# Performance work log

Hardware: AMD Instinct MI355X
Metric: run time of the kernel (lower is better)

The kernel has to match this reference:

```python
import jax, jax.numpy as jnp
import numpy as np

B, N, C1, C2, H = 4, 4096, 320, 256, 5
HD = C1 // H  # 64


def setup_inputs() -> dict:
    key = jax.random.key(0)
    ks = jax.random.split(key, 9)
    w = lambda k, shape, fan_in: jax.random.normal(k, shape, jnp.float32) * (fan_in ** -0.5)
    return {
        "x1": jax.random.normal(ks[0], (B, N, C1), jnp.float32),
        "x2": jax.random.normal(ks[1], (B, N, C2), jnp.float32),
        # nn.Linear weights, torch layout [out_features, in_features]
        "q1_w": w(ks[2], (C1, C1), C1),
        "q2_w": w(ks[3], (C1, C2), C2),
        "kv1_w": w(ks[4], (2 * C1, C2), C2),
        "kv2_w": w(ks[5], (2 * C1, C1), C1),
        "proj1_w": w(ks[6], (C1, C1), C1),
        "proj1_b": jnp.zeros((C1,), jnp.float32),
        "proj2_w": w(ks[7], (C1, C1), C1),
        "proj2_b": jnp.zeros((C1,), jnp.float32),
    }


def _branch(xq, xkv, q_w, kv_w, proj_w, proj_b):
    b, n, _ = xq.shape
    scale = HD ** -0.5
    q = (xq @ q_w.T).reshape(b, n, H, HD).transpose(0, 2, 1, 3)          # [B,H,N,HD]
    kv = (xkv @ kv_w.T).reshape(b, n, 2, H, HD).transpose(2, 0, 3, 1, 4)  # [2,B,H,N,HD]
    k, v = kv[0], kv[1]
    attn = jax.nn.softmax(jnp.einsum('bhqd,bhkd->bhqk', q * scale, k), axis=-1)
    y = jnp.einsum('bhqk,bhkd->bhqd', attn, v)                            # [B,H,N,HD]
    y = y.transpose(0, 2, 1, 3).reshape(b, n, C1)
    return y @ proj_w.T + proj_b


def reference(x1, x2, q1_w, q2_w, kv1_w, kv2_w, proj1_w, proj1_b, proj2_w, proj2_b):
    y1 = _branch(x1, x2, q1_w, kv1_w, proj1_w, proj1_b)  # x1 queries, x2 keys/values
    y2 = _branch(x2, x1, q2_w, kv2_w, proj2_w, proj2_b)  # x2 queries, x1 keys/values
    return jnp.concatenate((y1, y2), axis=-1)            # [B,N,2*C1]
```

## Files before the change

kernel.cpp:

```cpp
#include <hip/hip_runtime.h>
#include <hip/hip_bf16.h>

#define Bb 4
#define Nn 4096
#define C1 320
#define C2 256
#define Hh 5
#define HD 64
#define Mm (Bb*Nn)

using bf16 = __hip_bfloat16;
typedef __attribute__((ext_vector_type(8))) short  short8;
typedef __attribute__((ext_vector_type(4))) short  short4_;
typedef __attribute__((ext_vector_type(4))) float  f32x4;
typedef __attribute__((ext_vector_type(16))) float f32x16;
typedef __attribute__((ext_vector_type(2)))  float f32x2;

__device__ __forceinline__ short f2s(float f) {
    bf16 h = __float2bfloat16(f);
    short s;
    __builtin_memcpy(&s, &h, 2);
    return s;
}

__device__ __forceinline__ float fexp2(float x) {
#if __has_builtin(__builtin_amdgcn_exp2f)
    return __builtin_amdgcn_exp2f(x);
#else
    return exp2f(x);
#endif
}

__device__ __forceinline__ int swz(int row, int bb) {
    return row * 64 + ((bb ^ (row & 7)) << 3);
}
__device__ __forceinline__ int swz16(int row, int bb) {
    return row * 128 + ((bb ^ (row & 7)) << 3);
}

__device__ __forceinline__ unsigned cvtpk(float lo, float hi) {
    unsigned r;
    asm("v_cvt_pk_bf16_f32 %0, %1, %2" : "=v"(r) : "v"(lo), "v"(hi));
    return r;
}

__device__ __forceinline__ f32x2 pkadd(f32x2 a, f32x2 b) {
    f32x2 d;
    asm("v_pk_add_f32 %0, %1, %2" : "=v"(d) : "v"(a), "v"(b));
    return d;
}

__device__ __forceinline__ void plswap(unsigned &a, unsigned &b) {
#if __has_builtin(__builtin_amdgcn_permlane32_swap)
    auto r = __builtin_amdgcn_permlane32_swap(a, b, false, false);
    a = r[0]; b = r[1];
#else
    asm("v_permlane32_swap_b32 %0, %1" : "+v"(a), "+v"(b));
#endif
}

__device__ __forceinline__ short8 mk8(unsigned d0, unsigned d1, unsigned d2, unsigned d3) {
    union { unsigned u[4]; short8 s; } u;
    u.u[0] = d0; u.u[1] = d1; u.u[2] = d2; u.u[3] = d3;
    return u.s;
}

struct CvtArgs {
    const float* s[8];
    bf16* d[8];
    int off[9];
};

__global__ void cvt_all(CvtArgs a) {
    int i = (blockIdx.x * blockDim.x + threadIdx.x) * 4;
    if (i >= a.off[8]) return;
    int seg = 0;
    #pragma unroll
    for (int k = 1; k < 8; ++k) seg += (i >= a.off[k]);
    int j = i - a.off[seg];
    float4 v = *(const float4*)(a.s[seg] + j);
    short4_ o = { f2s(v.x), f2s(v.y), f2s(v.z), f2s(v.w) };
    *(short4_*)(a.d[seg] + j) = o;
}

__global__ __launch_bounds__(256) void gemm_proj(
    const bf16* __restrict__ A1, const bf16* __restrict__ Wq1, const bf16* __restrict__ Wkv1,
    const bf16* __restrict__ A2, const bf16* __restrict__ Wq2, const bf16* __restrict__ Wkv2,
    float qs,
    bf16* __restrict__ Qo1, bf16* __restrict__ Ko1, bf16* __restrict__ Vo1,
    bf16* __restrict__ Qo2, bf16* __restrict__ Ko2, bf16* __restrict__ Vo2)
{
    __shared__ bf16 la[128 * 64];
    __shared__ bf16 lw[64 * 64];
    const int m0 = blockIdx.x * 128;
    const int by = blockIdx.y;
    const int g = (by >= 15);
    const int yy = by - 15 * g;
    const int K = g ? C2 : C1;
    const bf16* A = g ? A2 : A1;
    const bool isq = yy < 5;
    const bf16* W = isq ? (g ? Wq2 : Wq1) : (g ? Wkv2 : Wkv1);
    bf16* Qo = g ? Qo2 : Qo1;
    bf16* Ko = g ? Ko2 : Ko1;
    bf16* Vo = g ? Vo2 : Vo1;
    const int n0 = (isq ? yy : yy - 5) * 64;
    const int t = threadIdx.x;
    const int wave = t >> 6, lane = t & 63, l16 = lane & 15, quad = lane >> 4;
    const int sr = t >> 3, sb = t & 7;

    f32x4 acc[2][4];
    #pragma unroll
    for (int mf = 0; mf < 2; ++mf)
        #pragma unroll
        for (int nt = 0; nt < 4; ++nt) acc[mf][nt] = {0.f,0.f,0.f,0.f};

    const int nk = K >> 6;
    const bf16* ap = A + (size_t)(m0 + sr) * K + sb * 8;
    const bf16* wp = W + (size_t)(n0 + sr) * K + sb * 8;
    short8 ra0 = *(const short8*)ap;
    short8 ra1 = *(const short8*)(ap + (size_t)32 * K);
    short8 ra2 = *(const short8*)(ap + (size_t)64 * K);
    short8 ra3 = *(const short8*)(ap + (size_t)96 * K);
    short8 rw0 = *(const short8*)wp;
    short8 rw1 = *(const short8*)(wp + (size_t)32 * K);

    for (int kt = 0; kt < nk; ++kt) {
        __syncthreads();
        *(short8*)&la[swz(sr,      sb)] = ra0;
        *(short8*)&la[swz(sr + 32, sb)] = ra1;
        *(short8*)&la[swz(sr + 64, sb)] = ra2;
        *(short8*)&la[swz(sr + 96, sb)] = ra3;
        *(short8*)&lw[swz(sr,      sb)] = rw0;
        *(short8*)&lw[swz(sr + 32, sb)] = rw1;
        __syncthreads();
        if (kt + 1 < nk) {
            ap += 64; wp += 64;
            ra0 = *(const short8*)ap;
            ra1 = *(const short8*)(ap + (size_t)32 * K);
            ra2 = *(const short8*)(ap + (size_t)64 * K);
            ra3 = *(const short8*)(ap + (size_t)96 * K);
            rw0 = *(const short8*)wp;
            rw1 = *(const short8*)(wp + (size_t)32 * K);
        }
        const int arow = wave * 32 + l16;
        short8 a00 = *(const short8*)&la[swz(arow,      quad)];
        short8 a01 = *(const short8*)&la[swz(arow,      quad + 4)];
        short8 a10 = *(const short8*)&la[swz(arow + 16, quad)];
        short8 a11 = *(const short8*)&la[swz(arow + 16, quad + 4)];
        #pragma unroll
        for (int nt = 0; nt < 4; ++nt) {
            const int brow = nt * 16 + l16;
            short8 b0 = *(const short8*)&lw[swz(brow, quad)];
            short8 b1 = *(const short8*)&lw[swz(brow, quad + 4)];
            acc[0][nt] = __builtin_amdgcn_mfma_f32_16x16x32_bf16(a00, b0, acc[0][nt], 0, 0, 0);
            acc[0][nt] = __builtin_amdgcn_mfma_f32_16x16x32_bf16(a01, b1, acc[0][nt], 0, 0, 0);
            acc[1][nt] = __builtin_amdgcn_mfma_f32_16x16x32_bf16(a10, b0, acc[1][nt], 0, 0, 0);
            acc[1][nt] = __builtin_amdgcn_mfma_f32_16x16x32_bf16(a11, b1, acc[1][nt], 0, 0, 0);
        }
    }

    const bool isv = !isq && n0 >= C1;
    #pragma unroll
    for (int mf = 0; mf < 2; ++mf) {
        const int mrow = m0 + wave * 32 + mf * 16 + quad * 4;
        if (isq) {
            #pragma unroll
            for (int nt = 0; nt < 4; ++nt) {
                int col = n0 + nt * 16 + l16;
                #pragma unroll
                for (int r = 0; r < 4; ++r)
                    Qo[(size_t)(mrow + r) * C1 + col] = __float2bfloat16(acc[mf][nt][r] * qs);
            }
        } else if (!isv) {
            #pragma unroll
            for (int nt = 0; nt < 4; ++nt) {
                int col = n0 + nt * 16 + l16;
                #pragma unroll
                for (int r = 0; r < 4; ++r)
                    Ko[(size_t)(mrow + r) * C1 + col] = __float2bfloat16(acc[mf][nt][r]);
            }
        } else {
            #pragma unroll
            for (int nt = 0; nt < 4; ++nt) {
                int col = n0 + nt * 16 + l16 - C1;
                int h = col >> 6, d = col & 63;
                #pragma unroll
                for (int r = 0; r < 4; ++r) {
                    int m = mrow + r;
                    int b = m >> 12, n = m & (Nn - 1);
                    Vo[((size_t)(b * Hh + h) * 64 + d) * Nn + n] = __float2bfloat16(acc[mf][nt][r]);
                }
            }
        }
    }
}

__global__ __launch_bounds__(256) void gemm_out(
    const bf16* __restrict__ Y1, const bf16* __restrict__ Wp1, const float* __restrict__ B1,
    const bf16* __restrict__ Y2, const bf16* __restrict__ Wp2, const float* __restrict__ B2,
    float* __restrict__ Of)
{
    __shared__ bf16 la[128 * 64];
    __shared__ bf16 lw[64 * 64];
    const int zz = blockIdx.z;
    const bf16* A = zz ? Y2 : Y1;
    const bf16* W = zz ? Wp2 : Wp1;
    const float* bias = zz ? B2 : B1;
    const int ooff = zz ? C1 : 0;
    const int m0 = blockIdx.x * 128, n0 = blockIdx.y * 64;
    const int t = threadIdx.x;
    const int wave = t >> 6, lane = t & 63, l16 = lane & 15, quad = lane >> 4;
    const int sr = t >> 3, sb = t & 7;
    const int K = C1;

    f32x4 acc[2][4];
    #pragma unroll
    for (int mf = 0; mf < 2; ++mf)
        #pragma unroll
        for (int nt = 0; nt < 4; ++nt) acc[mf][nt] = {0.f,0.f,0.f,0.f};

    const int nk = K >> 6;
    const bf16* ap = A + (size_t)(m0 + sr) * K + sb * 8;
    const bf16* wp = W + (size_t)(n0 + sr) * K + sb * 8;
    short8 ra0 = *(const short8*)ap;
    short8 ra1 = *(const short8*)(ap + (size_t)32 * K);
    short8 ra2 = *(const short8*)(ap + (size_t)64 * K);
    short8 ra3 = *(const short8*)(ap + (size_t)96 * K);
    short8 rw0 = *(const short8*)wp;
    short8 rw1 = *(const short8*)(wp + (size_t)32 * K);

    for (int kt = 0; kt < nk; ++kt) {
        __syncthreads();
        *(short8*)&la[swz(sr,      sb)] = ra0;
        *(short8*)&la[swz(sr + 32, sb)] = ra1;
        *(short8*)&la[swz(sr + 64, sb)] = ra2;
        *(short8*)&la[swz(sr + 96, sb)] = ra3;
        *(short8*)&lw[swz(sr,      sb)] = rw0;
        *(short8*)&lw[swz(sr + 32, sb)] = rw1;
        __syncthreads();
        if (kt + 1 < nk) {
            ap += 64; wp += 64;
            ra0 = *(const short8*)ap;
            ra1 = *(const short8*)(ap + (size_t)32 * K);
            ra2 = *(const short8*)(ap + (size_t)64 * K);
            ra3 = *(const short8*)(ap + (size_t)96 * K);
            rw0 = *(const short8*)wp;
            rw1 = *(const short8*)(wp + (size_t)32 * K);
        }
        const int arow = wave * 32 + l16;
        short8 a00 = *(const short8*)&la[swz(arow,      quad)];
        short8 a01 = *(const short8*)&la[swz(arow,      quad + 4)];
        short8 a10 = *(const short8*)&la[swz(arow + 16, quad)];
        short8 a11 = *(const short8*)&la[swz(arow + 16, quad + 4)];
        #pragma unroll
        for (int nt = 0; nt < 4; ++nt) {
            const int brow = nt * 16 + l16;
            short8 b0 = *(const short8*)&lw[swz(brow, quad)];
            short8 b1 = *(const short8*)&lw[swz(brow, quad + 4)];
            acc[0][nt] = __builtin_amdgcn_mfma_f32_16x16x32_bf16(a00, b0, acc[0][nt], 0, 0, 0);
            acc[0][nt] = __builtin_amdgcn_mfma_f32_16x16x32_bf16(a01, b1, acc[0][nt], 0, 0, 0);
            acc[1][nt] = __builtin_amdgcn_mfma_f32_16x16x32_bf16(a10, b0, acc[1][nt], 0, 0, 0);
            acc[1][nt] = __builtin_amdgcn_mfma_f32_16x16x32_bf16(a11, b1, acc[1][nt], 0, 0, 0);
        }
    }

    #pragma unroll
    for (int mf = 0; mf < 2; ++mf) {
        const int mrow = m0 + wave * 32 + mf * 16 + quad * 4;
        #pragma unroll
        for (int nt = 0; nt < 4; ++nt) {
            int col = n0 + nt * 16 + l16;
            float bv = bias[col];
            #pragma unroll
            for (int r = 0; r < 4; ++r)
                Of[(size_t)(mrow + r) * 640 + ooff + col] = acc[mf][nt][r] + bv;
        }
    }
}

__global__ __launch_bounds__(256, 2) void flash_kernel(
    const bf16* __restrict__ Q1, const bf16* __restrict__ K1,
    const bf16* __restrict__ V1, bf16* __restrict__ Y1,
    const bf16* __restrict__ Q2, const bf16* __restrict__ K2,
    const bf16* __restrict__ V2, bf16* __restrict__ Y2)
{
    __shared__ bf16 lk[128 * 64];
    __shared__ bf16 lv[64 * 128];
    const int qt = blockIdx.x, h = blockIdx.y, z = blockIdx.z;
    const int b = z & 3, branch = z >> 2;
    const bf16* Q  = branch ? Q2 : Q1;
    const bf16* Km = branch ? K2 : K1;
    const bf16* Vt = branch ? V2 : V1;
    bf16*       Yo = branch ? Y2 : Y1;

    const int t = threadIdx.x;
    const int wave = t >> 6, lane = t & 63;
    const int l32 = lane & 31, hi = lane >> 5;
    const int sr = t >> 3, sb = t & 7;

    const int qrow0 = qt * 256 + wave * 64;

    short8 qf[2][4];
    #pragma unroll
    for (int qb = 0; qb < 2; ++qb) {
        const bf16* qptr = Q + (size_t)(b * Nn + qrow0 + qb * 32 + l32) * C1 + h * HD + hi * 8;
        #pragma unroll
        for (int ksd = 0; ksd < 4; ++ksd)
            qf[qb][ksd] = *(const short8*)(qptr + ksd * 16);
    }

    f32x16 o[2][2];
    #pragma unroll
    for (int qb = 0; qb < 2; ++qb)
        #pragma unroll
        for (int db = 0; db < 2; ++db)
            o[qb][db] = (f32x16){0.f,0.f,0.f,0.f,0.f,0.f,0.f,0.f,0.f,0.f,0.f,0.f,0.f,0.f,0.f,0.f};
    float lsum[2] = {0.f, 0.f};

    const bf16* Kbase = Km + (size_t)b * Nn * C1 + h * HD;
    const bf16* Vbase = Vt + (size_t)(b * Hh + h) * 64 * Nn;

    const bf16* kp0 = Kbase + (size_t)sr * C1 + sb * 8;
    const bf16* vp0 = Vbase + (size_t)sr * Nn + sb * 8;
    short8 rk0 = *(const short8*)kp0;
    short8 rk1 = *(const short8*)(kp0 + (size_t)32 * C1);
    short8 rk2 = *(const short8*)(kp0 + (size_t)64 * C1);
    short8 rk3 = *(const short8*)(kp0 + (size_t)96 * C1);
    short8 rv0 = *(const short8*)vp0;
    short8 rv1 = *(const short8*)(vp0 + 64);
    short8 rv2 = *(const short8*)(vp0 + (size_t)32 * Nn);
    short8 rv3 = *(const short8*)(vp0 + (size_t)32 * Nn + 64);

    const int NT = Nn / 128;
    for (int kt = 0; kt < NT; ++kt) {
        __syncthreads();
        *(short8*)&lk[swz(sr,      sb)] = rk0;
        *(short8*)&lk[swz(sr + 32, sb)] = rk1;
        *(short8*)&lk[swz(sr + 64, sb)] = rk2;
        *(short8*)&lk[swz(sr + 96, sb)] = rk3;
        *(short8*)&lv[swz16(sr,      sb)]     = rv0;
        *(short8*)&lv[swz16(sr,      sb + 8)] = rv1;
        *(short8*)&lv[swz16(sr + 32, sb)]     = rv2;
        *(short8*)&lv[swz16(sr + 32, sb + 8)] = rv3;
        __syncthreads();
        if (kt + 1 < NT) {
            kp0 += (size_t)128 * C1;
            vp0 += 128;
            rk0 = *(const short8*)kp0;
            rk1 = *(const short8*)(kp0 + (size_t)32 * C1);
            rk2 = *(const short8*)(kp0 + (size_t)64 * C1);
            rk3 = *(const short8*)(kp0 + (size_t)96 * C1);
            rv0 = *(const short8*)vp0;
            rv1 = *(const short8*)(vp0 + 64);
            rv2 = *(const short8*)(vp0 + (size_t)32 * Nn);
            rv3 = *(const short8*)(vp0 + (size_t)32 * Nn + 64);
        }

        #pragma unroll
        for (int kb = 0; kb < 4; ++kb) {
            short8 ka[4];
            #pragma unroll
            for (int ksd = 0; ksd < 4; ++ksd)
                ka[ksd] = *(const short8*)&lk[swz(kb * 32 + l32, ksd * 2 + hi)];

            short8 pa[2][2];
            #pragma unroll
            for (int qb = 0; qb < 2; ++qb) {
                f32x16 s = (f32x16){0.f,0.f,0.f,0.f,0.f,0.f,0.f,0.f,0.f,0.f,0.f,0.f,0.f,0.f,0.f,0.f};
                #pragma unroll
                for (int ksd = 0; ksd < 4; ++ksd)
                    s = __builtin_amdgcn_mfma_f32_32x32x16_bf16(ka[ksd], qf[qb][ksd], s, 0, 0, 0);
                float p[16];
                #pragma unroll
                for (int r = 0; r < 16; ++r) p[r] = fexp2(s[r]);
                {
                    f32x2 t0 = pkadd((f32x2){p[0], p[1]},  (f32x2){p[2], p[3]});
                    f32x2 t1 = pkadd((f32x2){p[4], p[5]},  (f32x2){p[6], p[7]});
                    f32x2 t2 = pkadd((f32x2){p[8], p[9]},  (f32x2){p[10], p[11]});
                    f32x2 t3 = pkadd((f32x2){p[12], p[13]},(f32x2){p[14], p[15]});
                    t0 = pkadd(t0, t1);
                    t2 = pkadd(t2, t3);
                    t0 = pkadd(t0, t2);
                    lsum[qb] += t0.x + t0.y;
                }
                unsigned d0 = cvtpk(p[0],  p[1]),  d2 = cvtpk(p[4],  p[5]);
                plswap(d0, d2);
                unsigned d1 = cvtpk(p[2],  p[3]),  d3 = cvtpk(p[6],  p[7]);
                plswap(d1, d3);
                pa[qb][0] = mk8(d0, d1, d2, d3);
                unsigned e0 = cvtpk(p[8],  p[9]),  e2 = cvtpk(p[12], p[13]);
                plswap(e0, e2);
                unsigned e1 = cvtpk(p[10], p[11]), e3 = cvtpk(p[14], p[15]);
                plswap(e1, e3);
                pa[qb][1] = mk8(e0, e1, e2, e3);
            }

            #pragma unroll
            for (int ks = 0; ks < 2; ++ks) {
                #pragma unroll
                for (int db = 0; db < 2; ++db) {
                    short8 bv = *(const short8*)&lv[swz16(db * 32 + l32, kb * 4 + ks * 2 + hi)];
                    o[0][db] = __builtin_amdgcn_mfma_f32_32x32x16_bf16(pa[0][ks], bv, o[0][db], 0, 0, 0);
                    o[1][db] = __builtin_amdgcn_mfma_f32_32x32x16_bf16(pa[1][ks], bv, o[1][db], 0, 0, 0);
                }
            }
        }
    }

    #pragma unroll
    for (int qb = 0; qb < 2; ++qb) {
        float l = lsum[qb] + __shfl_xor(lsum[qb], 32, 64);
        float inv = 1.0f / l;
        #pragma unroll
        for (int r = 0; r < 16; ++r) {
            const int qr = (r & 3) + 8 * (r >> 2) + 4 * hi;
            float invr = __shfl(inv, qr, 64);
            size_t row = (size_t)(b * Nn + qrow0 + qb * 32 + qr);
            #pragma unroll
            for (int db = 0; db < 2; ++db)
                Yo[row * C1 + h * HD + db * 32 + l32] = __float2bfloat16(o[qb][db][r] * invr);
        }
    }
}

extern "C" void kernel_launch(void* const* d_in, const int* in_sizes, int n_in,
                              void* d_out, int out_size, void* d_ws, size_t ws_size,
                              hipStream_t stream)
{
    const float* x1   = (const float*)d_in[0];
    const float* x2   = (const float*)d_in[1];
    const float* q1w  = (const float*)d_in[2];
    const float* q2w  = (const float*)d_in[3];
    const float* kv1w = (const float*)d_in[4];
    const float* kv2w = (const float*)d_in[5];
    const float* p1w  = (const float*)d_in[6];
    const float* p1b  = (const float*)d_in[7];
    const float* p2w  = (const float*)d_in[8];
    const float* p2b  = (const float*)d_in[9];
    float* out = (float*)d_out;

    bf16* ws = (bf16*)d_ws;
    size_t o = 0;
    bf16* x1b  = ws + o; o += (size_t)Mm * C1;
    bf16* x2b  = ws + o; o += (size_t)Mm * C2;
    bf16* wq1  = ws + o; o += C1 * C1;
    bf16* wq2  = ws + o; o += C1 * C2;
    bf16* wkv1 = ws + o; o += 2 * C1 * C2;
    bf16* wkv2 = ws + o; o += 2 * C1 * C1;
    bf16* wp1  = ws + o; o += C1 * C1;
    bf16* wp2  = ws + o; o += C1 * C1;
    bf16* Q1   = ws + o; o += (size_t)Mm * C1;
    bf16* K1   = ws + o; o += (size_t)Mm * C1;
    bf16* V1t  = ws + o; o += (size_t)Mm * C1;
    bf16* Q2   = ws + o; o += (size_t)Mm * C1;
    bf16* K2   = ws + o; o += (size_t)Mm * C1;
    bf16* V2t  = ws + o; o += (size_t)Mm * C1;
    bf16* Y1   = ws + o; o += (size_t)Mm * C1;
    bf16* Y2   = ws + o; o += (size_t)Mm * C1;
    (void)ws_size; (void)in_sizes; (void)n_in; (void)out_size;

    CvtArgs ca;
    ca.s[0] = x1;   ca.d[0] = x1b;  int n0 = Mm * C1;
    ca.s[1] = x2;   ca.d[1] = x2b;  int n1 = Mm * C2;
    ca.s[2] = q1w;  ca.d[2] = wq1;  int n2 = C1 * C1;
    ca.s[3] = q2w;  ca.d[3] = wq2;  int n3 = C1 * C2;
    ca.s[4] = kv1w; ca.d[4] = wkv1; int n4 = 2 * C1 * C2;
    ca.s[5] = kv2w; ca.d[5] = wkv2; int n5 = 2 * C1 * C1;
    ca.s[6] = p1w;  ca.d[6] = wp1;  int n6 = C1 * C1;
    ca.s[7] = p2w;  ca.d[7] = wp2;  int n7 = C1 * C1;
    int ns[8] = {n0, n1, n2, n3, n4, n5, n6, n7};
    ca.off[0] = 0;
    for (int i = 0; i < 8; ++i) ca.off[i + 1] = ca.off[i] + ns[i];
    int total = ca.off[8];
    cvt_all<<<dim3((total / 4 + 255) / 256), 256, 0, stream>>>(ca);

    const float QS = 0.125f * 1.4426950408889634f;

    gemm_proj<<<dim3(Mm / 128, 30), 256, 0, stream>>>(
        x1b, wq1, wkv2, x2b, wq2, wkv1, QS,
        Q1, K2, V2t, Q2, K1, V1t);

    flash_kernel<<<dim3(Nn / 256, Hh, 2 * Bb), 256, 0, stream>>>(Q1, K1, V1t, Y1, Q2, K2, V2t, Y2);

    gemm_out<<<dim3(Mm / 128, C1 / 64, 2), 256, 0, stream>>>(Y1, wp1, p1b, Y2, wp2, p2b, out);
}
```

Before: 352.2 us.

## Fuse activation fp32-to-bf16 conversion into projection GEMM; shrink flash KV tile

The projection GEMM now loads the fp32 activations directly and converts them to bf16 in registers before the shared-memory store, so the separate conversion pass over x1/x2 and its bf16 workspace copies go away. The conversion kernel now handles only the weights. Separately, the flash attention kernel's K/V tile drops from 128 to 64 keys per iteration, halving shared memory and prefetch registers in exchange for twice as many barrier-synchronised iterations. The GEMM now reads twice as many bytes of A per tile, and because gemm_proj has 30 column blocks per row panel, the fp32 activations are fetched repeatedly at double width.

```diff
diff --git a/kernel.cpp b/kernel.cpp
--- a/kernel.cpp
+++ b/kernel.cpp
@@ -34,9 +34,6 @@
 __device__ __forceinline__ int swz(int row, int bb) {
     return row * 64 + ((bb ^ (row & 7)) << 3);
 }
-__device__ __forceinline__ int swz16(int row, int bb) {
-    return row * 128 + ((bb ^ (row & 7)) << 3);
-}
 
 __device__ __forceinline__ unsigned cvtpk(float lo, float hi) {
     unsigned r;
@@ -65,18 +62,23 @@
     return u.s;
 }
 
+__device__ __forceinline__ short8 cvt8(float4 lo, float4 hi) {
+    return mk8(cvtpk(lo.x, lo.y), cvtpk(lo.z, lo.w),
+               cvtpk(hi.x, hi.y), cvtpk(hi.z, hi.w));
+}
+
 struct CvtArgs {
-    const float* s[8];
-    bf16* d[8];
-    int off[9];
+    const float* s[6];
+    bf16* d[6];
+    int off[7];
 };
 
 __global__ void cvt_all(CvtArgs a) {
     int i = (blockIdx.x * blockDim.x + threadIdx.x) * 4;
-    if (i >= a.off[8]) return;
+    if (i >= a.off[6]) return;
     int seg = 0;
     #pragma unroll
-    for (int k = 1; k < 8; ++k) seg += (i >= a.off[k]);
+    for (int k = 1; k < 6; ++k) seg += (i >= a.off[k]);
     int j = i - a.off[seg];
     float4 v = *(const float4*)(a.s[seg] + j);
     short4_ o = { f2s(v.x), f2s(v.y), f2s(v.z), f2s(v.w) };
@@ -84,8 +86,8 @@
 }
 
 __global__ __launch_bounds__(256) void gemm_proj(
-    const bf16* __restrict__ A1, const bf16* __restrict__ Wq1, const bf16* __restrict__ Wkv1,
-    const bf16* __restrict__ A2, const bf16* __restrict__ Wq2, const bf16* __restrict__ Wkv2,
+    const float* __restrict__ A1, const bf16* __restrict__ Wq1, const bf16* __restrict__ Wkv1,
+    const float* __restrict__ A2, const bf16* __restrict__ Wq2, const bf16* __restrict__ Wkv2,
     float qs,
     bf16* __restrict__ Qo1, bf16* __restrict__ Ko1, bf16* __restrict__ Vo1,
     bf16* __restrict__ Qo2, bf16* __restrict__ Ko2, bf16* __restrict__ Vo2)
@@ -97,7 +99,7 @@
     const int g = (by >= 15);
     const int yy = by - 15 * g;
     const int K = g ? C2 : C1;
-    const bf16* A = g ? A2 : A1;
+    const float* A = g ? A2 : A1;
     const bool isq = yy < 5;
     const bf16* W = isq ? (g ? Wq2 : Wq1) : (g ? Wkv2 : Wkv1);
     bf16* Qo = g ? Qo2 : Qo1;
@@ -115,30 +117,30 @@
         for (int nt = 0; nt < 4; ++nt) acc[mf][nt] = {0.f,0.f,0.f,0.f};
 
     const int nk = K >> 6;
-    const bf16* ap = A + (size_t)(m0 + sr) * K + sb * 8;
-    const bf16* wp = W + (size_t)(n0 + sr) * K + sb * 8;
-    short8 ra0 = *(const short8*)ap;
-    short8 ra1 = *(const short8*)(ap + (size_t)32 * K);
-    short8 ra2 = *(const short8*)(ap + (size_t)64 * K);
-    short8 ra3 = *(const short8*)(ap + (size_t)96 * K);
+    const float* ap = A + (size_t)(m0 + sr) * K + sb * 8;
+    const bf16*  wp = W + (size_t)(n0 + sr) * K + sb * 8;
+    float4 fa0 = *(const float4*)ap,                       fa0h = *(const float4*)(ap + 4);
+    float4 fa1 = *(const float4*)(ap + (size_t)32 * K),    fa1h = *(const float4*)(ap + (size_t)32 * K + 4);
+    float4 fa2 = *(const float4*)(ap + (size_t)64 * K),    fa2h = *(const float4*)(ap + (size_t)64 * K + 4);
+    float4 fa3 = *(const float4*)(ap + (size_t)96 * K),    fa3h = *(const float4*)(ap + (size_t)96 * K + 4);
     short8 rw0 = *(const short8*)wp;
     short8 rw1 = *(const short8*)(wp + (size_t)32 * K);
 
     for (int kt = 0; kt < nk; ++kt) {
         __syncthreads();
-        *(short8*)&la[swz(sr,      sb)] = ra0;
-        *(short8*)&la[swz(sr + 32, sb)] = ra1;
-        *(short8*)&la[swz(sr + 64, sb)] = ra2;
-        *(short8*)&la[swz(sr + 96, sb)] = ra3;
+        *(short8*)&la[swz(sr,      sb)] = cvt8(fa0, fa0h);
+        *(short8*)&la[swz(sr + 32, sb)] = cvt8(fa1, fa1h);
+        *(short8*)&la[swz(sr + 64, sb)] = cvt8(fa2, fa2h);
+        *(short8*)&la[swz(sr + 96, sb)] = cvt8(fa3, fa3h);
         *(short8*)&lw[swz(sr,      sb)] = rw0;
         *(short8*)&lw[swz(sr + 32, sb)] = rw1;
         __syncthreads();
         if (kt + 1 < nk) {
             ap += 64; wp += 64;
-            ra0 = *(const short8*)ap;
-            ra1 = *(const short8*)(ap + (size_t)32 * K);
-            ra2 = *(const short8*)(ap + (size_t)64 * K);
-            ra3 = *(const short8*)(ap + (size_t)96 * K);
+            fa0 = *(const float4*)ap;                    fa0h = *(const float4*)(ap + 4);
+            fa1 = *(const float4*)(ap + (size_t)32 * K); fa1h = *(const float4*)(ap + (size_t)32 * K + 4);
+            fa2 = *(const float4*)(ap + (size_t)64 * K); fa2h = *(const float4*)(ap + (size_t)64 * K + 4);
+            fa3 = *(const float4*)(ap + (size_t)96 * K); fa3h = *(const float4*)(ap + (size_t)96 * K + 4);
             rw0 = *(const short8*)wp;
             rw1 = *(const short8*)(wp + (size_t)32 * K);
         }
@@ -284,8 +286,8 @@
     const bf16* __restrict__ Q2, const bf16* __restrict__ K2,
     const bf16* __restrict__ V2, bf16* __restrict__ Y2)
 {
-    __shared__ bf16 lk[128 * 64];
-    __shared__ bf16 lv[64 * 128];
+    __shared__ bf16 lk[64 * 64];
+    __shared__ bf16 lv[64 * 64];
     const int qt = blockIdx.x, h = blockIdx.y, z = blockIdx.z;
     const int b = z & 3, branch = z >> 2;
     const bf16* Q  = branch ? Q2 : Q1;
@@ -321,43 +323,32 @@
     const bf16* Vbase = Vt + (size_t)(b * Hh + h) * 64 * Nn;
 
     const bf16* kp0 = Kbase + (size_t)sr * C1 + sb * 8;
+    const bf16* kp1 = kp0 + (size_t)32 * C1;
     const bf16* vp0 = Vbase + (size_t)sr * Nn + sb * 8;
+    const bf16* vp1 = vp0 + (size_t)32 * Nn;
     short8 rk0 = *(const short8*)kp0;
-    short8 rk1 = *(const short8*)(kp0 + (size_t)32 * C1);
-    short8 rk2 = *(const short8*)(kp0 + (size_t)64 * C1);
-    short8 rk3 = *(const short8*)(kp0 + (size_t)96 * C1);
+    short8 rk1 = *(const short8*)kp1;
     short8 rv0 = *(const short8*)vp0;
-    short8 rv1 = *(const short8*)(vp0 + 64);
-    short8 rv2 = *(const short8*)(vp0 + (size_t)32 * Nn);
-    short8 rv3 = *(const short8*)(vp0 + (size_t)32 * Nn + 64);
-
-    const int NT = Nn / 128;
+    short8 rv1 = *(const short8*)vp1;
+
+    const int NT = Nn / 64;
     for (int kt = 0; kt < NT; ++kt) {
         __syncthreads();
-        *(short8*)&lk[swz(sr,      sb)] = rk0;
+        *(short8*)&lk[swz(sr, sb)]      = rk0;
         *(short8*)&lk[swz(sr + 32, sb)] = rk1;
-        *(short8*)&lk[swz(sr + 64, sb)] = rk2;
-        *(short8*)&lk[swz(sr + 96, sb)] = rk3;
-        *(short8*)&lv[swz16(sr,      sb)]     = rv0;
-        *(short8*)&lv[swz16(sr,      sb + 8)] = rv1;
-        *(short8*)&lv[swz16(sr + 32, sb)]     = rv2;
-        *(short8*)&lv[swz16(sr + 32, sb + 8)] = rv3;
+        *(short8*)&lv[swz(sr, sb)]      = rv0;
+        *(short8*)&lv[swz(sr + 32, sb)] = rv1;
         __syncthreads();
         if (kt + 1 < NT) {
-            kp0 += (size_t)128 * C1;
-            vp0 += 128;
+            kp0 += 64 * C1; kp1 += 64 * C1; vp0 += 64; vp1 += 64;
             rk0 = *(const short8*)kp0;
-            rk1 = *(const short8*)(kp0 + (size_t)32 * C1);
-            rk2 = *(const short8*)(kp0 + (size_t)64 * C1);
-            rk3 = *(const short8*)(kp0 + (size_t)96 * C1);
+            rk1 = *(const short8*)kp1;
             rv0 = *(const short8*)vp0;
-            rv1 = *(const short8*)(vp0 + 64);
-            rv2 = *(const short8*)(vp0 + (size_t)32 * Nn);
-            rv3 = *(const short8*)(vp0 + (size_t)32 * Nn + 64);
-        }
-
-        #pragma unroll
-        for (int kb = 0; kb < 4; ++kb) {
+            rv1 = *(const short8*)vp1;
+        }
+
+        #pragma unroll
+        for (int kb = 0; kb < 2; ++kb) {
             short8 ka[4];
             #pragma unroll
             for (int ksd = 0; ksd < 4; ++ksd)
@@ -399,7 +390,7 @@
             for (int ks = 0; ks < 2; ++ks) {
                 #pragma unroll
                 for (int db = 0; db < 2; ++db) {
-                    short8 bv = *(const short8*)&lv[swz16(db * 32 + l32, kb * 4 + ks * 2 + hi)];
+                    short8 bv = *(const short8*)&lv[swz(db * 32 + l32, kb * 4 + ks * 2 + hi)];
                     o[0][db] = __builtin_amdgcn_mfma_f32_32x32x16_bf16(pa[0][ks], bv, o[0][db], 0, 0, 0);
                     o[1][db] = __builtin_amdgcn_mfma_f32_32x32x16_bf16(pa[1][ks], bv, o[1][db], 0, 0, 0);
                 }
@@ -441,8 +432,6 @@
 
     bf16* ws = (bf16*)d_ws;
     size_t o = 0;
-    bf16* x1b  = ws + o; o += (size_t)Mm * C1;
-    bf16* x2b  = ws + o; o += (size_t)Mm * C2;
     bf16* wq1  = ws + o; o += C1 * C1;
     bf16* wq2  = ws + o; o += C1 * C2;
     bf16* wkv1 = ws + o; o += 2 * C1 * C2;
@@ -460,24 +449,22 @@
     (void)ws_size; (void)in_sizes; (void)n_in; (void)out_size;
 
     CvtArgs ca;
-    ca.s[0] = x1;   ca.d[0] = x1b;  int n0 = Mm * C1;
-    ca.s[1] = x2;   ca.d[1] = x2b;  int n1 = Mm * C2;
-    ca.s[2] = q1w;  ca.d[2] = wq1;  int n2 = C1 * C1;
-    ca.s[3] = q2w;  ca.d[3] = wq2;  int n3 = C1 * C2;
-    ca.s[4] = kv1w; ca.d[4] = wkv1; int n4 = 2 * C1 * C2;
-    ca.s[5] = kv2w; ca.d[5] = wkv2; int n5 = 2 * C1 * C1;
-    ca.s[6] = p1w;  ca.d[6] = wp1;  int n6 = C1 * C1;
-    ca.s[7] = p2w;  ca.d[7] = wp2;  int n7 = C1 * C1;
-    int ns[8] = {n0, n1, n2, n3, n4, n5, n6, n7};
+    ca.s[0] = q1w;  ca.d[0] = wq1;  int n0 = C1 * C1;
+    ca.s[1] = q2w;  ca.d[1] = wq2;  int n1 = C1 * C2;
+    ca.s[2] = kv1w; ca.d[2] = wkv1; int n2 = 2 * C1 * C2;
+    ca.s[3] = kv2w; ca.d[3] = wkv2; int n3 = 2 * C1 * C1;
+    ca.s[4] = p1w;  ca.d[4] = wp1;  int n4 = C1 * C1;
+    ca.s[5] = p2w;  ca.d[5] = wp2;  int n5 = C1 * C1;
+    int ns[6] = {n0, n1, n2, n3, n4, n5};
     ca.off[0] = 0;
-    for (int i = 0; i < 8; ++i) ca.off[i + 1] = ca.off[i] + ns[i];
-    int total = ca.off[8];
+    for (int i = 0; i < 6; ++i) ca.off[i + 1] = ca.off[i] + ns[i];
+    int total = ca.off[6];
     cvt_all<<<dim3((total / 4 + 255) / 256), 256, 0, stream>>>(ca);
 
     const float QS = 0.125f * 1.4426950408889634f;
 
     gemm_proj<<<dim3(Mm / 128, 30), 256, 0, stream>>>(
-        x1b, wq1, wkv2, x2b, wq2, wkv1, QS,
+        x1, wq1, wkv2, x2, wq2, wkv1, QS,
         Q1, K2, V2t, Q2, K1, V1t);
 
     flash_kernel<<<dim3(Nn / 256, Hh, 2 * Bb), 256, 0, stream>>>(Q1, K1, V1t, Y1, Q2, K2, V2t, Y2);
```

After: 344.0 us. -2.3%, faster.
